# Kernel optimization log

Hardware: AMD Instinct MI355X
Metric: run time of the kernel (lower is better)

Reference implementation:

```python
import jax, jax.numpy as jnp
import numpy as np

N_FULL = 50000
N_POOL = 12500
E_FULL = 600000
E_POOL = 150000
D = 128


def gcn_conv(x, W, b, edge_index, n):
    """GCNConv with self-loops and symmetric normalization.
    x: [n, d_in], W: [d_in, d_out], edge_index: [2, E] (src -> dst)."""
    xw = x @ W  # [n, d_out]
    loops = jnp.arange(n, dtype=edge_index.dtype)
    src = jnp.concatenate([edge_index[0], loops])
    dst = jnp.concatenate([edge_index[1], loops])
    deg = jnp.zeros((n,), dtype=xw.dtype).at[dst].add(1.0)  # >= 1 (self loops)
    dinv = jax.lax.rsqrt(deg)
    norm = (dinv[src] * dinv[dst])[:, None]  # [E+n, 1]
    out = jax.ops.segment_sum(xw[src] * norm, dst, num_segments=n)
    return out + b


def setup_inputs() -> dict:
    key = jax.random.key(0)
    ks = jax.random.split(key, 8)
    s = 1.0 / np.sqrt(D)
    return {
        "x": jnp.zeros((N_FULL, D), jnp.float32),
        "edge_index": jax.random.randint(ks[0], (2, E_FULL), 0, N_FULL, dtype=jnp.int64)
            if jax.config.jax_enable_x64 else jax.random.randint(ks[0], (2, E_FULL), 0, N_FULL).astype(jnp.int32),
        "pooled_x": jax.random.normal(ks[1], (N_POOL, D), jnp.float32),
        "pooled_edge_index": jax.random.randint(ks[2], (2, E_POOL), 0, N_POOL).astype(jnp.int32),
        "unpool_info": jnp.arange(N_POOL, dtype=jnp.int32),  # unique TopK-kept indices
        "W0": jax.random.normal(ks[3], (D, D), jnp.float32) * s,
        "b0": jnp.zeros((D,), jnp.float32),
        "W1": jax.random.normal(ks[4], (D, D), jnp.float32) * s,
        "b1": jnp.zeros((D,), jnp.float32),
        "W2": jax.random.normal(ks[5], (D, D), jnp.float32) * s,
        "b2": jnp.zeros((D,), jnp.float32),
    }


def reference(x, edge_index, pooled_x, pooled_edge_index, unpool_info,
              W0, b0, W1, b1, W2, b2):
    n = x.shape[0]
    # conv0 on the pooled graph + activation (ELU)
    h = jax.nn.elu(gcn_conv(pooled_x, W0, b0, pooled_edge_index, pooled_x.shape[0]))
    # TopKPool unpool: zero full graph, scatter pooled features to kept indices
    xf = jnp.zeros_like(x).at[unpool_info].set(h)
    # remaining convs on the full graph (dropout=0 / eval mode -> identity)
    xf = jax.nn.elu(gcn_conv(xf, W1, b1, edge_index, n))
    xf = jax.nn.elu(gcn_conv(xf, W2, b2, edge_index, n))
    return xf
```

## Files before the change

kernel.cpp:

```cpp
#include <hip/hip_runtime.h>
#include <math.h>

#define DD 128
#define CF 48
#define C1 16
#define OVF_CAP 4096

static inline int cdiv(long a, long b){ return (int)((a + b - 1) / b); }

typedef __attribute__((ext_vector_type(4))) float f32x4;
typedef __attribute__((ext_vector_type(8))) short bf16x8;
typedef __attribute__((ext_vector_type(4))) short sh4;

__device__ __forceinline__ unsigned short bf16_rn(float f){
  unsigned u = __float_as_uint(f);
  u += 0x7fffu + ((u >> 16) & 1u);
  return (unsigned short)(u >> 16);
}

__global__ void k_count(const int* __restrict__ dst_f, int Ef, int* __restrict__ cnt_f,
                        int* __restrict__ rank_f,
                        const int* __restrict__ dst_p, int Ep, int* __restrict__ cnt_p,
                        int* __restrict__ rank_p,
                        const int* __restrict__ unpool, int* __restrict__ invm, int npool){
  int e = blockIdx.x * blockDim.x + threadIdx.x;
  if (e < Ef){ rank_f[e] = atomicAdd(&cnt_f[dst_f[e]], 1); return; }
  e -= Ef;
  if (e < Ep){ rank_p[e] = atomicAdd(&cnt_p[dst_p[e]], 1); return; }
  e -= Ep;
  if (e < npool) invm[unpool[e]] = e + 1;
}

__global__ void k_fill(const int* __restrict__ src_f, const int* __restrict__ dst_f, int Ef,
                       const int* __restrict__ cnt_f, const int* __restrict__ rank_f,
                       const int* __restrict__ invm,
                       unsigned* __restrict__ ew2, int4* __restrict__ ovf2, int* __restrict__ novf2,
                       int* __restrict__ rk1, unsigned* __restrict__ ew1,
                       int4* __restrict__ ovf1, int* __restrict__ novf1,
                       const int* __restrict__ src_p, const int* __restrict__ dst_p, int Ep,
                       const int* __restrict__ cnt_p, const int* __restrict__ rank_p,
                       unsigned* __restrict__ ew0, int4* __restrict__ ovf0, int* __restrict__ novf0){
  int e = blockIdx.x * blockDim.x + threadIdx.x;
  if (e < Ef){
    int s = src_f[e], d = dst_f[e], r = rank_f[e];
    int c = cnt_f[s]; c = c < 255 ? c : 255;
    unsigned u = ((unsigned)s << 8) | (unsigned)c;
    if (r < CF) ew2[(long)d * CF + r] = u;
    else { int o = atomicAdd(novf2, 1); if (o < OVF_CAP) ovf2[o] = make_int4(s, c, d, 0); }
    int pv = invm[s];
    if (pv > 0){
      int pr = pv - 1;
      int r1 = atomicAdd(&rk1[d], 1);
      unsigned u1 = ((unsigned)pr << 8) | (unsigned)c;
      if (r1 < C1) ew1[(long)d * C1 + r1] = u1;
      else { int o = atomicAdd(novf1, 1); if (o < OVF_CAP) ovf1[o] = make_int4(pr, c, d, 0); }
    }
    return;
  }
  e -= Ef;
  if (e < Ep){
    int s = src_p[e], d = dst_p[e], r = rank_p[e];
    int c = cnt_p[s]; c = c < 255 ? c : 255;
    unsigned u = ((unsigned)s << 8) | (unsigned)c;
    if (r < CF) ew0[(long)d * CF + r] = u;
    else { int o = atomicAdd(novf0, 1); if (o < OVF_CAP) ovf0[o] = make_int4(s, c, d, 0); }
  }
}

template <int AMODE, bool BF16OUT>
__global__ __launch_bounds__(256, 2) void k_gemm_mfma(const void* __restrict__ Ap,
                                                      const float* __restrict__ W,
                                                      void* __restrict__ Cout, int n){
  __shared__ unsigned short Wl[2][16384];
  const int t    = threadIdx.x;
  const int lane = t & 63;
  const int wv   = t >> 6;
  const int g    = lane >> 4;
  const int r    = lane & 15;

  #pragma unroll
  for (int i = 0; i < 4; i++){
    int item = t + i * 256;
    int kq = item >> 5;
    int c4 = item & 31;
    const float* Wp = W + (long)kq * 512 + c4 * 4;
    float4 ww[4];
    #pragma unroll
    for (int kk = 0; kk < 4; kk++) ww[kk] = *(const float4*)(Wp + kk * 128);
    #pragma unroll
    for (int m = 0; m < 4; m++){
      int c = c4 * 4 + m;
      int boff = c * 256 + (((kq >> 1) ^ (c & 15)) * 16) + (kq & 1) * 8;
      sh4 hq, lq;
      #pragma unroll
      for (int kk = 0; kk < 4; kk++){
        float f = ((const float*)&ww[kk])[m];
        unsigned short hh = bf16_rn(f);
        float hf = __uint_as_float((unsigned)hh << 16);
        hq[kk] = (short)hh;
        lq[kk] = (short)bf16_rn(f - hf);
      }
      *(sh4*)((char*)(&Wl[0][0]) + boff) = hq;
      *(sh4*)((char*)(&Wl[1][0]) + boff) = lq;
    }
  }
  __syncthreads();

  const int rb = blockIdx.x * 128 + wv * 32;
  const int r0 = rb + r, r1 = rb + 16 + r;
  const bool v0 = r0 < n, v1 = r1 < n;

  f32x4 acc[2][8];
  #pragma unroll
  for (int i = 0; i < 2; i++)
    #pragma unroll
    for (int j = 0; j < 8; j++){ f32x4 z = {0.f,0.f,0.f,0.f}; acc[i][j] = z; }

  #pragma unroll
  for (int ks = 0; ks < 4; ks++){
    bf16x8 ah0, al0, ah1, al1;
    if (AMODE == 0){
      const float* pa0 = (const float*)Ap + (long)r0 * DD + g * 8;
      const float* pa1 = (const float*)Ap + (long)r1 * DD + g * 8;
      const float4 z4 = make_float4(0.f,0.f,0.f,0.f);
      float4 a00 = v0 ? *(const float4*)(pa0 + ks * 32)     : z4;
      float4 a01 = v0 ? *(const float4*)(pa0 + ks * 32 + 4) : z4;
      float4 a10 = v1 ? *(const float4*)(pa1 + ks * 32)     : z4;
      float4 a11 = v1 ? *(const float4*)(pa1 + ks * 32 + 4) : z4;
      float f0[8] = {a00.x,a00.y,a00.z,a00.w,a01.x,a01.y,a01.z,a01.w};
      float f1[8] = {a10.x,a10.y,a10.z,a10.w,a11.x,a11.y,a11.z,a11.w};
      #pragma unroll
      for (int i = 0; i < 8; i++){
        unsigned short hh = bf16_rn(f0[i]);
        ah0[i] = (short)hh;
        al0[i] = (short)bf16_rn(f0[i] - __uint_as_float((unsigned)hh << 16));
        unsigned short h1 = bf16_rn(f1[i]);
        ah1[i] = (short)h1;
        al1[i] = (short)bf16_rn(f1[i] - __uint_as_float((unsigned)h1 << 16));
      }
    } else {
      const unsigned* qa0 = (const unsigned*)Ap + (long)r0 * DD + g * 8;
      const unsigned* qa1 = (const unsigned*)Ap + (long)r1 * DD + g * 8;
      const uint4 z4 = make_uint4(0,0,0,0);
      uint4 u00 = v0 ? *(const uint4*)(qa0 + ks * 32)     : z4;
      uint4 u01 = v0 ? *(const uint4*)(qa0 + ks * 32 + 4) : z4;
      uint4 u10 = v1 ? *(const uint4*)(qa1 + ks * 32)     : z4;
      uint4 u11 = v1 ? *(const uint4*)(qa1 + ks * 32 + 4) : z4;
      unsigned uu0[8] = {u00.x,u00.y,u00.z,u00.w,u01.x,u01.y,u01.z,u01.w};
      unsigned uu1[8] = {u10.x,u10.y,u10.z,u10.w,u11.x,u11.y,u11.z,u11.w};
      #pragma unroll
      for (int i = 0; i < 8; i++){
        ah0[i] = (short)(uu0[i] & 0xffffu); al0[i] = (short)(uu0[i] >> 16);
        ah1[i] = (short)(uu1[i] & 0xffffu); al1[i] = (short)(uu1[i] >> 16);
      }
    }
    const int sb = ks * 4 + g;
    #pragma unroll
    for (int cf = 0; cf < 8; cf++){
      const int boff = (cf * 16 + r) * 256 + ((sb ^ r) * 16);
      bf16x8 wh = *(const bf16x8*)((const char*)(&Wl[0][0]) + boff);
      bf16x8 wl = *(const bf16x8*)((const char*)(&Wl[1][0]) + boff);
      acc[0][cf] = __builtin_amdgcn_mfma_f32_16x16x32_bf16(ah0, wh, acc[0][cf], 0, 0, 0);
      acc[1][cf] = __builtin_amdgcn_mfma_f32_16x16x32_bf16(ah1, wh, acc[1][cf], 0, 0, 0);
      acc[0][cf] = __builtin_amdgcn_mfma_f32_16x16x32_bf16(al0, wh, acc[0][cf], 0, 0, 0);
      acc[1][cf] = __builtin_amdgcn_mfma_f32_16x16x32_bf16(al1, wh, acc[1][cf], 0, 0, 0);
      acc[0][cf] = __builtin_amdgcn_mfma_f32_16x16x32_bf16(ah0, wl, acc[0][cf], 0, 0, 0);
      acc[1][cf] = __builtin_amdgcn_mfma_f32_16x16x32_bf16(ah1, wl, acc[1][cf], 0, 0, 0);
    }
  }

  #pragma unroll
  for (int rf = 0; rf < 2; rf++){
    #pragma unroll
    for (int cf = 0; cf < 8; cf++){
      #pragma unroll
      for (int e = 0; e < 4; e++){
        int row = rb + rf * 16 + g * 4 + e;
        if (row < n){
          float v = acc[rf][cf][e];
          if (BF16OUT)
            ((unsigned short*)Cout)[(long)row * DD + cf * 16 + r] = bf16_rn(v);
          else
            ((float*)Cout)[(long)row * DD + cf * 16 + r] = v;
        }
      }
    }
  }
}

__global__ __launch_bounds__(256) void k_agg0(const float* __restrict__ xw,
    const int* __restrict__ cnt, const unsigned* __restrict__ ew,
    const int4* __restrict__ ovf, const int* __restrict__ novf,
    const float* __restrict__ b, unsigned* __restrict__ outp, int n){
  int row = blockIdx.x * 4 + (threadIdx.x >> 6);
  if (row >= n) return;
  int c = (threadIdx.x & 63) * 2;
  int deg = __builtin_amdgcn_readfirstlane(cnt[row]);
  int m = deg < CF ? deg : CF;
  long base = (long)row * CF;
  float ax[4], ay[4];
  #pragma unroll
  for (int i = 0; i < 4; i++){ ax[i] = 0.f; ay[i] = 0.f; }
  int j = 0;
  for (; j + 3 < m; j += 4){
    uint4 q = *(const uint4*)(ew + base + j);
    unsigned ua[4] = {q.x, q.y, q.z, q.w};
    #pragma unroll
    for (int i = 0; i < 4; i++){
      int s = (int)(ua[i] >> 8);
      float w = rsqrtf((float)(ua[i] & 255u) + 1.f);
      float2 v = *(const float2*)(xw + (long)s * DD + c);
      ax[i] += v.x * w; ay[i] += v.y * w;
    }
  }
  for (; j < m; j++){
    unsigned u = ew[base + j];
    int s = (int)(u >> 8);
    float w = rsqrtf((float)(u & 255u) + 1.f);
    float2 v = *(const float2*)(xw + (long)s * DD + c);
    ax[0] += v.x * w; ay[0] += v.y * w;
  }
  int no = __builtin_amdgcn_readfirstlane(novf[0]);
  if (no > 0){
    no = no < OVF_CAP ? no : OVF_CAP;
    for (int k = 0; k < no; k++){
      int4 od = ovf[k];
      if (od.z == row){
        float w = rsqrtf((float)od.y + 1.f);
        float2 v = *(const float2*)(xw + (long)od.x * DD + c);
        ax[0] += v.x * w; ay[0] += v.y * w;
      }
    }
  }
  float sax = (ax[0]+ax[1]) + (ax[2]+ax[3]);
  float say = (ay[0]+ay[1]) + (ay[2]+ay[3]);
  float dd = rsqrtf((float)deg + 1.f);
  float2 sv = *(const float2*)(xw + (long)row * DD + c);
  float2 bb = *(const float2*)(b + c);
  float vx = sax * dd + sv.x * dd * dd + bb.x;
  float vy = say * dd + sv.y * dd * dd + bb.y;
  vx = vx > 0.f ? vx : expm1f(vx);
  vy = vy > 0.f ? vy : expm1f(vy);
  unsigned short hx = bf16_rn(vx);
  unsigned short lx = bf16_rn(vx - __uint_as_float((unsigned)hx << 16));
  unsigned short hy = bf16_rn(vy);
  unsigned short ly = bf16_rn(vy - __uint_as_float((unsigned)hy << 16));
  *(uint2*)(outp + (long)row * DD + c) =
      make_uint2((unsigned)hx | ((unsigned)lx << 16), (unsigned)hy | ((unsigned)ly << 16));
}

__global__ __launch_bounds__(256) void k_agg1(const unsigned short* __restrict__ hwb,
    const int* __restrict__ invm, const int* __restrict__ cnt_f,
    const int* __restrict__ rk1, const unsigned* __restrict__ ew,
    const int4* __restrict__ ovf, const int* __restrict__ novf,
    const float* __restrict__ b, unsigned* __restrict__ outp, int n){
  int row = blockIdx.x * 4 + (threadIdx.x >> 6);
  if (row >= n) return;
  int c = (threadIdx.x & 63) * 2;
  int m1 = __builtin_amdgcn_readfirstlane(rk1[row]);
  if (m1 > C1) m1 = C1;
  int deg = __builtin_amdgcn_readfirstlane(cnt_f[row]);
  long base = (long)row * C1;
  float ax[4], ay[4];
  #pragma unroll
  for (int i = 0; i < 4; i++){ ax[i] = 0.f; ay[i] = 0.f; }
  int j = 0;
  for (; j + 3 < m1; j += 4){
    uint4 q = *(const uint4*)(ew + base + j);
    unsigned ua[4] = {q.x, q.y, q.z, q.w};
    #pragma unroll
    for (int i = 0; i < 4; i++){
      int pr = (int)(ua[i] >> 8);
      float w = rsqrtf((float)(ua[i] & 255u) + 1.f);
      unsigned v = *(const unsigned*)(hwb + (long)pr * DD + c);
      ax[i] += __uint_as_float(v << 16) * w;
      ay[i] += __uint_as_float(v & 0xffff0000u) * w;
    }
  }
  for (; j < m1; j++){
    unsigned u = ew[base + j];
    int pr = (int)(u >> 8);
    float w = rsqrtf((float)(u & 255u) + 1.f);
    unsigned v = *(const unsigned*)(hwb + (long)pr * DD + c);
    ax[0] += __uint_as_float(v << 16) * w;
    ay[0] += __uint_as_float(v & 0xffff0000u) * w;
  }
  int no = __builtin_amdgcn_readfirstlane(novf[0]);
  if (no > 0){
    no = no < OVF_CAP ? no : OVF_CAP;
    for (int k = 0; k < no; k++){
      int4 od = ovf[k];
      if (od.z == row){
        float w = rsqrtf((float)od.y + 1.f);
        unsigned v = *(const unsigned*)(hwb + (long)od.x * DD + c);
        ax[0] += __uint_as_float(v << 16) * w;
        ay[0] += __uint_as_float(v & 0xffff0000u) * w;
      }
    }
  }
  float sax = (ax[0]+ax[1]) + (ax[2]+ax[3]);
  float say = (ay[0]+ay[1]) + (ay[2]+ay[3]);
  float dd = rsqrtf((float)deg + 1.f);
  int pv = invm[row];
  float sx = 0.f, sy = 0.f;
  if (pv > 0){
    unsigned sv = *(const unsigned*)(hwb + (long)(pv - 1) * DD + c);
    sx = __uint_as_float(sv << 16); sy = __uint_as_float(sv & 0xffff0000u);
  }
  float2 bb = *(const float2*)(b + c);
  float vx = sax * dd + sx * dd * dd + bb.x;
  float vy = say * dd + sy * dd * dd + bb.y;
  vx = vx > 0.f ? vx : expm1f(vx);
  vy = vy > 0.f ? vy : expm1f(vy);
  unsigned short hx = bf16_rn(vx);
  unsigned short lx = bf16_rn(vx - __uint_as_float((unsigned)hx << 16));
  unsigned short hy = bf16_rn(vy);
  unsigned short ly = bf16_rn(vy - __uint_as_float((unsigned)hy << 16));
  *(uint2*)(outp + (long)row * DD + c) =
      make_uint2((unsigned)hx | ((unsigned)lx << 16), (unsigned)hy | ((unsigned)ly << 16));
}

__global__ __launch_bounds__(256) void k_agg2(const unsigned short* __restrict__ xwb,
    const int* __restrict__ cnt, const unsigned* __restrict__ ew,
    const int4* __restrict__ ovf, const int* __restrict__ novf,
    const float* __restrict__ b, float* __restrict__ out, int n){
  int row = blockIdx.x * 4 + (threadIdx.x >> 6);
  if (row >= n) return;
  int c = (threadIdx.x & 63) * 2;
  int deg = __builtin_amdgcn_readfirstlane(cnt[row]);
  int m = deg < CF ? deg : CF;
  long base = (long)row * CF;
  float ax[8], ay[8];
  #pragma unroll
  for (int i = 0; i < 8; i++){ ax[i] = 0.f; ay[i] = 0.f; }
  int j = 0;
  for (; j + 7 < m; j += 8){
    uint4 q0 = *(const uint4*)(ew + base + j);
    uint4 q1 = *(const uint4*)(ew + base + j + 4);
    unsigned ua[8] = {q0.x, q0.y, q0.z, q0.w, q1.x, q1.y, q1.z, q1.w};
    #pragma unroll
    for (int i = 0; i < 8; i++){
      int s = (int)(ua[i] >> 8);
      float w = rsqrtf((float)(ua[i] & 255u) + 1.f);
      unsigned v = *(const unsigned*)(xwb + (long)s * DD + c);
      ax[i] += __uint_as_float(v << 16) * w;
      ay[i] += __uint_as_float(v & 0xffff0000u) * w;
    }
  }
  for (; j < m; j++){
    unsigned u = ew[base + j];
    int s = (int)(u >> 8);
    float w = rsqrtf((float)(u & 255u) + 1.f);
    unsigned v = *(const unsigned*)(xwb + (long)s * DD + c);
    ax[0] += __uint_as_float(v << 16) * w;
    ay[0] += __uint_as_float(v & 0xffff0000u) * w;
  }
  int no = __builtin_amdgcn_readfirstlane(novf[0]);
  if (no > 0){
    no = no < OVF_CAP ? no : OVF_CAP;
    for (int k = 0; k < no; k++){
      int4 od = ovf[k];
      if (od.z == row){
        float w = rsqrtf((float)od.y + 1.f);
        unsigned v = *(const unsigned*)(xwb + (long)od.x * DD + c);
        ax[0] += __uint_as_float(v << 16) * w;
        ay[0] += __uint_as_float(v & 0xffff0000u) * w;
      }
    }
  }
  float sax = ((ax[0]+ax[1])+(ax[2]+ax[3])) + ((ax[4]+ax[5])+(ax[6]+ax[7]));
  float say = ((ay[0]+ay[1])+(ay[2]+ay[3])) + ((ay[4]+ay[5])+(ay[6]+ay[7]));
  float dd = rsqrtf((float)deg + 1.f);
  unsigned sv = *(const unsigned*)(xwb + (long)row * DD + c);
  float sx = __uint_as_float(sv << 16), sy = __uint_as_float(sv & 0xffff0000u);
  float2 bb = *(const float2*)(b + c);
  float vx = sax * dd + sx * dd * dd + bb.x;
  float vy = say * dd + sy * dd * dd + bb.y;
  vx = vx > 0.f ? vx : expm1f(vx);
  vy = vy > 0.f ? vy : expm1f(vy);
  *(float2*)(out + (long)row * DD + c) = make_float2(vx, vy);
}

extern "C" void kernel_launch(void* const* d_in, const int* in_sizes, int n_in,
                              void* d_out, int out_size, void* d_ws, size_t ws_size,
                              hipStream_t stream) {
  const int*   edge   = (const int*)d_in[1];
  const float* px     = (const float*)d_in[2];
  const int*   pedge  = (const int*)d_in[3];
  const int*   unpool = (const int*)d_in[4];
  const float* W0 = (const float*)d_in[5]; const float* b0 = (const float*)d_in[6];
  const float* W1 = (const float*)d_in[7]; const float* b1 = (const float*)d_in[8];
  const float* W2 = (const float*)d_in[9]; const float* b2 = (const float*)d_in[10];
  const int n_full = in_sizes[0] / DD;
  const int E_full = in_sizes[1] / 2;
  const int n_pool = in_sizes[2] / DD;
  const int E_pool = in_sizes[3] / 2;
  float* out = (float*)d_out;

  char* w = (char*)d_ws;
  size_t off = 0;
  auto alloc = [&](size_t bytes) -> void* {
    void* p = (void*)(w + off);
    off += (bytes + 255) / 256 * 256;
    return p;
  };
  int* cnt_f = (int*)alloc((size_t)n_full * 4);
  int* cnt_p = (int*)alloc((size_t)n_pool * 4);
  int* rk1   = (int*)alloc((size_t)n_full * 4);
  int* novf3 = (int*)alloc(12);
  int* invm  = (int*)alloc((size_t)n_full * 4);
  size_t zspan = (size_t)((char*)(invm + n_full) - (char*)cnt_f);
  int* rank_f = (int*)alloc((size_t)E_full * 4);
  int* rank_p = (int*)alloc((size_t)E_pool * 4);
  unsigned* ew2 = (unsigned*)alloc((size_t)n_full * CF * 4);
  unsigned* ew1 = (unsigned*)alloc((size_t)n_full * C1 * 4);
  unsigned* ew0 = (unsigned*)alloc((size_t)n_pool * CF * 4);
  int4* ovf2 = (int4*)alloc((size_t)OVF_CAP * 16);
  int4* ovf1 = (int4*)alloc((size_t)OVF_CAP * 16);
  int4* ovf0 = (int4*)alloc((size_t)OVF_CAP * 16);
  const size_t big = (size_t)n_full * DD * 4;
  float* bufA = (float*)alloc(big);
  float* bufB = (float*)alloc(big);

  const int* src_f = edge;          const int* dst_f = edge + E_full;
  const int* src_p = pedge;         const int* dst_p = pedge + E_pool;

  (void)hipMemsetAsync(cnt_f, 0, zspan, stream);
  k_count<<<cdiv((long)E_full + E_pool + n_pool, 256), 256, 0, stream>>>(
      dst_f, E_full, cnt_f, rank_f, dst_p, E_pool, cnt_p, rank_p, unpool, invm, n_pool);
  k_fill<<<cdiv((long)E_full + E_pool, 256), 256, 0, stream>>>(
      src_f, dst_f, E_full, cnt_f, rank_f, invm,
      ew2, ovf2, novf3 + 0,
      rk1, ew1, ovf1, novf3 + 1,
      src_p, dst_p, E_pool, cnt_p, rank_p,
      ew0, ovf0, novf3 + 2);

  float* xw0            = bufA;
  unsigned* h0p         = (unsigned*)bufB;
  unsigned short* hw1b  = (unsigned short*)bufA;
  unsigned* y1p         = (unsigned*)bufB;
  unsigned short* xw2b  = (unsigned short*)bufA;

  k_gemm_mfma<0,false><<<cdiv(n_pool,128),256,0,stream>>>(px, W0, xw0, n_pool);
  k_agg0<<<cdiv(n_pool,4),256,0,stream>>>(xw0, cnt_p, ew0, ovf0, novf3 + 2, b0, h0p, n_pool);

  k_gemm_mfma<1,true><<<cdiv(n_pool,128),256,0,stream>>>(h0p, W1, hw1b, n_pool);
  k_agg1<<<cdiv(n_full,4),256,0,stream>>>(hw1b, invm, cnt_f, rk1, ew1, ovf1, novf3 + 1, b1, y1p, n_full);

  k_gemm_mfma<1,true><<<cdiv(n_full,128),256,0,stream>>>(y1p, W2, xw2b, n_full);
  k_agg2<<<cdiv(n_full,4),256,0,stream>>>(xw2b, cnt_f, ew2, ovf2, novf3 + 0, b2, out, n_full);
}
```

Measured before the change: 268.5 us.

## Vectorize edge count/fill kernels and batch 16 gathers per aggregation step

The count and fill preprocessing kernels now have each thread handle four edges with int4 loads of src/dst/rank, which cuts thread count and widens memory accesses. The aggregation kernels load 16 packed edge entries at once and issue all 16 feature gathers before accumulating, using predicated weights instead of scalar tail loops, to raise memory-level parallelism. Row index and invm are made wave-uniform via readfirstlane. The cost is wasted gathers on padded slots and higher register pressure. It also relies on the padded edge rows being readable past the valid count and on 16-byte alignment of the edge arrays.

```diff
diff --git a/kernel.cpp b/kernel.cpp
--- a/kernel.cpp
+++ b/kernel.cpp
@@ -18,30 +18,91 @@
   return (unsigned short)(u >> 16);
 }
 
-__global__ void k_count(const int* __restrict__ dst_f, int Ef, int* __restrict__ cnt_f,
-                        int* __restrict__ rank_f,
-                        const int* __restrict__ dst_p, int Ep, int* __restrict__ cnt_p,
-                        int* __restrict__ rank_p,
+__global__ void k_count(const int* __restrict__ dst_f, int nF4, int Ef,
+                        int* __restrict__ cnt_f, int* __restrict__ rank_f,
+                        const int* __restrict__ dst_p, int nP4, int Ep,
+                        int* __restrict__ cnt_p, int* __restrict__ rank_p,
                         const int* __restrict__ unpool, int* __restrict__ invm, int npool){
-  int e = blockIdx.x * blockDim.x + threadIdx.x;
-  if (e < Ef){ rank_f[e] = atomicAdd(&cnt_f[dst_f[e]], 1); return; }
-  e -= Ef;
-  if (e < Ep){ rank_p[e] = atomicAdd(&cnt_p[dst_p[e]], 1); return; }
-  e -= Ep;
-  if (e < npool) invm[unpool[e]] = e + 1;
-}
-
-__global__ void k_fill(const int* __restrict__ src_f, const int* __restrict__ dst_f, int Ef,
+  int t = blockIdx.x * blockDim.x + threadIdx.x;
+  if (t < nF4){
+    int e = t * 4;
+    int4 d = *(const int4*)(dst_f + e);
+    int r0 = atomicAdd(&cnt_f[d.x], 1);
+    int r1 = atomicAdd(&cnt_f[d.y], 1);
+    int r2 = atomicAdd(&cnt_f[d.z], 1);
+    int r3 = atomicAdd(&cnt_f[d.w], 1);
+    *(int4*)(rank_f + e) = make_int4(r0, r1, r2, r3);
+    return;
+  }
+  t -= nF4;
+  int remF = Ef - nF4 * 4;
+  if (t < remF){ int e = nF4 * 4 + t; rank_f[e] = atomicAdd(&cnt_f[dst_f[e]], 1); return; }
+  t -= remF;
+  if (t < nP4){
+    int e = t * 4;
+    int4 d = *(const int4*)(dst_p + e);
+    int r0 = atomicAdd(&cnt_p[d.x], 1);
+    int r1 = atomicAdd(&cnt_p[d.y], 1);
+    int r2 = atomicAdd(&cnt_p[d.z], 1);
+    int r3 = atomicAdd(&cnt_p[d.w], 1);
+    *(int4*)(rank_p + e) = make_int4(r0, r1, r2, r3);
+    return;
+  }
+  t -= nP4;
+  int remP = Ep - nP4 * 4;
+  if (t < remP){ int e = nP4 * 4 + t; rank_p[e] = atomicAdd(&cnt_p[dst_p[e]], 1); return; }
+  t -= remP;
+  if (t < npool) invm[unpool[t]] = t + 1;
+}
+
+__global__ void k_fill(const int* __restrict__ src_f, const int* __restrict__ dst_f,
+                       int nF4, int Ef,
                        const int* __restrict__ cnt_f, const int* __restrict__ rank_f,
                        const int* __restrict__ invm,
                        unsigned* __restrict__ ew2, int4* __restrict__ ovf2, int* __restrict__ novf2,
                        int* __restrict__ rk1, unsigned* __restrict__ ew1,
                        int4* __restrict__ ovf1, int* __restrict__ novf1,
-                       const int* __restrict__ src_p, const int* __restrict__ dst_p, int Ep,
+                       const int* __restrict__ src_p, const int* __restrict__ dst_p,
+                       int nP4, int Ep,
                        const int* __restrict__ cnt_p, const int* __restrict__ rank_p,
                        unsigned* __restrict__ ew0, int4* __restrict__ ovf0, int* __restrict__ novf0){
-  int e = blockIdx.x * blockDim.x + threadIdx.x;
-  if (e < Ef){
+  int t = blockIdx.x * blockDim.x + threadIdx.x;
+  if (t < nF4){
+    int e = t * 4;
+    int4 s4 = *(const int4*)(src_f + e);
+    int4 d4 = *(const int4*)(dst_f + e);
+    int4 r4 = *(const int4*)(rank_f + e);
+    int sa[4] = {s4.x, s4.y, s4.z, s4.w};
+    int da[4] = {d4.x, d4.y, d4.z, d4.w};
+    int ra[4] = {r4.x, r4.y, r4.z, r4.w};
+    int ca[4], pa[4];
+    #pragma unroll
+    for (int i = 0; i < 4; i++){
+      int c = cnt_f[sa[i]]; ca[i] = c < 255 ? c : 255;
+      pa[i] = invm[sa[i]];
+    }
+    #pragma unroll
+    for (int i = 0; i < 4; i++){
+      unsigned u = ((unsigned)sa[i] << 8) | (unsigned)ca[i];
+      if (ra[i] < CF) ew2[(long)da[i] * CF + ra[i]] = u;
+      else { int o = atomicAdd(novf2, 1); if (o < OVF_CAP) ovf2[o] = make_int4(sa[i], ca[i], da[i], 0); }
+    }
+    #pragma unroll
+    for (int i = 0; i < 4; i++){
+      if (pa[i] > 0){
+        int pr = pa[i] - 1;
+        int r1 = atomicAdd(&rk1[da[i]], 1);
+        unsigned u1 = ((unsigned)pr << 8) | (unsigned)ca[i];
+        if (r1 < C1) ew1[(long)da[i] * C1 + r1] = u1;
+        else { int o = atomicAdd(novf1, 1); if (o < OVF_CAP) ovf1[o] = make_int4(pr, ca[i], da[i], 0); }
+      }
+    }
+    return;
+  }
+  t -= nF4;
+  int remF = Ef - nF4 * 4;
+  if (t < remF){
+    int e = nF4 * 4 + t;
     int s = src_f[e], d = dst_f[e], r = rank_f[e];
     int c = cnt_f[s]; c = c < 255 ? c : 255;
     unsigned u = ((unsigned)s << 8) | (unsigned)c;
@@ -57,8 +118,30 @@
     }
     return;
   }
-  e -= Ef;
-  if (e < Ep){
+  t -= remF;
+  if (t < nP4){
+    int e = t * 4;
+    int4 s4 = *(const int4*)(src_p + e);
+    int4 d4 = *(const int4*)(dst_p + e);
+    int4 r4 = *(const int4*)(rank_p + e);
+    int sa[4] = {s4.x, s4.y, s4.z, s4.w};
+    int da[4] = {d4.x, d4.y, d4.z, d4.w};
+    int ra[4] = {r4.x, r4.y, r4.z, r4.w};
+    int ca[4];
+    #pragma unroll
+    for (int i = 0; i < 4; i++){ int c = cnt_p[sa[i]]; ca[i] = c < 255 ? c : 255; }
+    #pragma unroll
+    for (int i = 0; i < 4; i++){
+      unsigned u = ((unsigned)sa[i] << 8) | (unsigned)ca[i];
+      if (ra[i] < CF) ew0[(long)da[i] * CF + ra[i]] = u;
+      else { int o = atomicAdd(novf0, 1); if (o < OVF_CAP) ovf0[o] = make_int4(sa[i], ca[i], da[i], 0); }
+    }
+    return;
+  }
+  t -= nP4;
+  int remP = Ep - nP4 * 4;
+  if (t < remP){
+    int e = nP4 * 4 + t;
     int s = src_p[e], d = dst_p[e], r = rank_p[e];
     int c = cnt_p[s]; c = c < 255 ? c : 255;
     unsigned u = ((unsigned)s << 8) | (unsigned)c;
@@ -192,33 +275,35 @@
     const int* __restrict__ cnt, const unsigned* __restrict__ ew,
     const int4* __restrict__ ovf, const int* __restrict__ novf,
     const float* __restrict__ b, unsigned* __restrict__ outp, int n){
-  int row = blockIdx.x * 4 + (threadIdx.x >> 6);
+  int row = __builtin_amdgcn_readfirstlane(blockIdx.x * 4 + (threadIdx.x >> 6));
   if (row >= n) return;
   int c = (threadIdx.x & 63) * 2;
   int deg = __builtin_amdgcn_readfirstlane(cnt[row]);
   int m = deg < CF ? deg : CF;
   long base = (long)row * CF;
-  float ax[4], ay[4];
-  #pragma unroll
-  for (int i = 0; i < 4; i++){ ax[i] = 0.f; ay[i] = 0.f; }
-  int j = 0;
-  for (; j + 3 < m; j += 4){
-    uint4 q = *(const uint4*)(ew + base + j);
-    unsigned ua[4] = {q.x, q.y, q.z, q.w};
-    #pragma unroll
-    for (int i = 0; i < 4; i++){
-      int s = (int)(ua[i] >> 8);
-      float w = rsqrtf((float)(ua[i] & 255u) + 1.f);
-      float2 v = *(const float2*)(xw + (long)s * DD + c);
-      ax[i] += v.x * w; ay[i] += v.y * w;
-    }
-  }
-  for (; j < m; j++){
-    unsigned u = ew[base + j];
-    int s = (int)(u >> 8);
-    float w = rsqrtf((float)(u & 255u) + 1.f);
-    float2 v = *(const float2*)(xw + (long)s * DD + c);
-    ax[0] += v.x * w; ay[0] += v.y * w;
+  float ax[8], ay[8];
+  #pragma unroll
+  for (int i = 0; i < 8; i++){ ax[i] = 0.f; ay[i] = 0.f; }
+  for (int j0 = 0; j0 < m; j0 += 16){
+    uint4 q0 = *(const uint4*)(ew + base + j0);
+    uint4 q1 = *(const uint4*)(ew + base + j0 + 4);
+    uint4 q2 = *(const uint4*)(ew + base + j0 + 8);
+    uint4 q3 = *(const uint4*)(ew + base + j0 + 12);
+    unsigned ua[16] = {q0.x,q0.y,q0.z,q0.w, q1.x,q1.y,q1.z,q1.w,
+                       q2.x,q2.y,q2.z,q2.w, q3.x,q3.y,q3.z,q3.w};
+    float2 v[16]; float w[16];
+    #pragma unroll
+    for (int i = 0; i < 16; i++){
+      bool val = (j0 + i) < m;
+      int s = val ? (int)(ua[i] >> 8) : row;
+      w[i] = val ? rsqrtf((float)(ua[i] & 255u) + 1.f) : 0.f;
+      v[i] = *(const float2*)(xw + (long)s * DD + c);
+    }
+    #pragma unroll
+    for (int i = 0; i < 16; i++){
+      ax[i & 7] += v[i].x * w[i];
+      ay[i & 7] += v[i].y * w[i];
+    }
   }
   int no = __builtin_amdgcn_readfirstlane(novf[0]);
   if (no > 0){
@@ -232,8 +317,8 @@
       }
     }
   }
-  float sax = (ax[0]+ax[1]) + (ax[2]+ax[3]);
-  float say = (ay[0]+ay[1]) + (ay[2]+ay[3]);
+  float sax = ((ax[0]+ax[1])+(ax[2]+ax[3])) + ((ax[4]+ax[5])+(ax[6]+ax[7]));
+  float say = ((ay[0]+ay[1])+(ay[2]+ay[3])) + ((ay[4]+ay[5])+(ay[6]+ay[7]));
   float dd = rsqrtf((float)deg + 1.f);
   float2 sv = *(const float2*)(xw + (long)row * DD + c);
   float2 bb = *(const float2*)(b + c);
@@ -254,36 +339,37 @@
     const int* __restrict__ rk1, const unsigned* __restrict__ ew,
     const int4* __restrict__ ovf, const int* __restrict__ novf,
     const float* __restrict__ b, unsigned* __restrict__ outp, int n){
-  int row = blockIdx.x * 4 + (threadIdx.x >> 6);
+  int row = __builtin_amdgcn_readfirstlane(blockIdx.x * 4 + (threadIdx.x >> 6));
   if (row >= n) return;
   int c = (threadIdx.x & 63) * 2;
   int m1 = __builtin_amdgcn_readfirstlane(rk1[row]);
   if (m1 > C1) m1 = C1;
   int deg = __builtin_amdgcn_readfirstlane(cnt_f[row]);
   long base = (long)row * C1;
-  float ax[4], ay[4];
-  #pragma unroll
-  for (int i = 0; i < 4; i++){ ax[i] = 0.f; ay[i] = 0.f; }
-  int j = 0;
-  for (; j + 3 < m1; j += 4){
-    uint4 q = *(const uint4*)(ew + base + j);
-    unsigned ua[4] = {q.x, q.y, q.z, q.w};
-    #pragma unroll
-    for (int i = 0; i < 4; i++){
-      int pr = (int)(ua[i] >> 8);
-      float w = rsqrtf((float)(ua[i] & 255u) + 1.f);
-      unsigned v = *(const unsigned*)(hwb + (long)pr * DD + c);
-      ax[i] += __uint_as_float(v << 16) * w;
-      ay[i] += __uint_as_float(v & 0xffff0000u) * w;
-    }
-  }
-  for (; j < m1; j++){
-    unsigned u = ew[base + j];
-    int pr = (int)(u >> 8);
-    float w = rsqrtf((float)(u & 255u) + 1.f);
-    unsigned v = *(const unsigned*)(hwb + (long)pr * DD + c);
-    ax[0] += __uint_as_float(v << 16) * w;
-    ay[0] += __uint_as_float(v & 0xffff0000u) * w;
+  int pv = __builtin_amdgcn_readfirstlane(invm[row]);
+  float ax[8], ay[8];
+  #pragma unroll
+  for (int i = 0; i < 8; i++){ ax[i] = 0.f; ay[i] = 0.f; }
+  if (m1 > 0){
+    uint4 q0 = *(const uint4*)(ew + base);
+    uint4 q1 = *(const uint4*)(ew + base + 4);
+    uint4 q2 = *(const uint4*)(ew + base + 8);
+    uint4 q3 = *(const uint4*)(ew + base + 12);
+    unsigned ua[16] = {q0.x,q0.y,q0.z,q0.w, q1.x,q1.y,q1.z,q1.w,
+                       q2.x,q2.y,q2.z,q2.w, q3.x,q3.y,q3.z,q3.w};
+    unsigned v[16]; float w[16];
+    #pragma unroll
+    for (int i = 0; i < 16; i++){
+      bool val = i < m1;
+      int pr = val ? (int)(ua[i] >> 8) : 0;
+      w[i] = val ? rsqrtf((float)(ua[i] & 255u) + 1.f) : 0.f;
+      v[i] = *(const unsigned*)(hwb + (long)pr * DD + c);
+    }
+    #pragma unroll
+    for (int i = 0; i < 16; i++){
+      ax[i & 7] += __uint_as_float(v[i] << 16) * w[i];
+      ay[i & 7] += __uint_as_float(v[i] & 0xffff0000u) * w[i];
+    }
   }
   int no = __builtin_amdgcn_readfirstlane(novf[0]);
   if (no > 0){
@@ -298,10 +384,9 @@
       }
     }
   }
-  float sax = (ax[0]+ax[1]) + (ax[2]+ax[3]);
-  float say = (ay[0]+ay[1]) + (ay[2]+ay[3]);
+  float sax = ((ax[0]+ax[1])+(ax[2]+ax[3])) + ((ax[4]+ax[5])+(ax[6]+ax[7]));
+  float say = ((ay[0]+ay[1])+(ay[2]+ay[3])) + ((ay[4]+ay[5])+(ay[6]+ay[7]));
   float dd = rsqrtf((float)deg + 1.f);
-  int pv = invm[row];
   float sx = 0.f, sy = 0.f;
   if (pv > 0){
     unsigned sv = *(const unsigned*)(hwb + (long)(pv - 1) * DD + c);
@@ -324,7 +409,7 @@
     const int* __restrict__ cnt, const unsigned* __restrict__ ew,
     const int4* __restrict__ ovf, const int* __restrict__ novf,
     const float* __restrict__ b, float* __restrict__ out, int n){
-  int row = blockIdx.x * 4 + (threadIdx.x >> 6);
+  int row = __builtin_amdgcn_readfirstlane(blockIdx.x * 4 + (threadIdx.x >> 6));
   if (row >= n) return;
   int c = (threadIdx.x & 63) * 2;
   int deg = __builtin_amdgcn_readfirstlane(cnt[row]);
@@ -333,27 +418,26 @@
   float ax[8], ay[8];
   #pragma unroll
   for (int i = 0; i < 8; i++){ ax[i] = 0.f; ay[i] = 0.f; }
-  int j = 0;
-  for (; j + 7 < m; j += 8){
-    uint4 q0 = *(const uint4*)(ew + base + j);
-    uint4 q1 = *(const uint4*)(ew + base + j + 4);
-    unsigned ua[8] = {q0.x, q0.y, q0.z, q0.w, q1.x, q1.y, q1.z, q1.w};
-    #pragma unroll
-    for (int i = 0; i < 8; i++){
-      int s = (int)(ua[i] >> 8);
-      float w = rsqrtf((float)(ua[i] & 255u) + 1.f);
-      unsigned v = *(const unsigned*)(xwb + (long)s * DD + c);
-      ax[i] += __uint_as_float(v << 16) * w;
-      ay[i] += __uint_as_float(v & 0xffff0000u) * w;
-    }
-  }
-  for (; j < m; j++){
-    unsigned u = ew[base + j];
-    int s = (int)(u >> 8);
-    float w = rsqrtf((float)(u & 255u) + 1.f);
-    unsigned v = *(const unsigned*)(xwb + (long)s * DD + c);
-    ax[0] += __uint_as_float(v << 16) * w;
-    ay[0] += __uint_as_float(v & 0xffff0000u) * w;
+  for (int j0 = 0; j0 < m; j0 += 16){
+    uint4 q0 = *(const uint4*)(ew + base + j0);
+    uint4 q1 = *(const uint4*)(ew + base + j0 + 4);
+    uint4 q2 = *(const uint4*)(ew + base + j0 + 8);
+    uint4 q3 = *(const uint4*)(ew + base + j0 + 12);
+    unsigned ua[16] = {q0.x,q0.y,q0.z,q0.w, q1.x,q1.y,q1.z,q1.w,
+                       q2.x,q2.y,q2.z,q2.w, q3.x,q3.y,q3.z,q3.w};
+    unsigned v[16]; float w[16];
+    #pragma unroll
+    for (int i = 0; i < 16; i++){
+      bool val = (j0 + i) < m;
+      int s = val ? (int)(ua[i] >> 8) : row;
+      w[i] = val ? rsqrtf((float)(ua[i] & 255u) + 1.f) : 0.f;
+      v[i] = *(const unsigned*)(xwb + (long)s * DD + c);
+    }
+    #pragma unroll
+    for (int i = 0; i < 16; i++){
+      ax[i & 7] += __uint_as_float(v[i] << 16) * w[i];
+      ay[i & 7] += __uint_as_float(v[i] & 0xffff0000u) * w[i];
+    }
   }
   int no = __builtin_amdgcn_readfirstlane(novf[0]);
   if (no > 0){
@@ -425,14 +509,19 @@
   const int* src_f = edge;          const int* dst_f = edge + E_full;
   const int* src_p = pedge;         const int* dst_p = pedge + E_pool;
 
+  const int nF4 = E_full / 4, remF = E_full & 3;
+  const int nP4 = E_pool / 4, remP = E_pool & 3;
+
   (void)hipMemsetAsync(cnt_f, 0, zspan, stream);
-  k_count<<<cdiv((long)E_full + E_pool + n_pool, 256), 256, 0, stream>>>(
-      dst_f, E_full, cnt_f, rank_f, dst_p, E_pool, cnt_p, rank_p, unpool, invm, n_pool);
-  k_fill<<<cdiv((long)E_full + E_pool, 256), 256, 0, stream>>>(
-      src_f, dst_f, E_full, cnt_f, rank_f, invm,
+  k_count<<<cdiv((long)nF4 + remF + nP4 + remP + n_pool, 256), 256, 0, stream>>>(
+      dst_f, nF4, E_full, cnt_f, rank_f,
+      dst_p, nP4, E_pool, cnt_p, rank_p,
+      unpool, invm, n_pool);
+  k_fill<<<cdiv((long)nF4 + remF + nP4 + remP, 256), 256, 0, stream>>>(
+      src_f, dst_f, nF4, E_full, cnt_f, rank_f, invm,
       ew2, ovf2, novf3 + 0,
       rk1, ew1, ovf1, novf3 + 1,
-      src_p, dst_p, E_pool, cnt_p, rank_p,
+      src_p, dst_p, nP4, E_pool, cnt_p, rank_p,
       ew0, ovf0, novf3 + 2);
 
   float* xw0            = bufA;
```

After: 262.7 us, median of 2. 1.02x faster.
